# Kernel optimization log

Measured on AMD Instinct MI355X. Metric: run time of the kernel, lower is better.

Reference implementation:

```python
import jax, jax.numpy as jnp
import numpy as np

HIDDEN = 4096
HALF = HIDDEN // 2
THRESH = 0.85


def setup_inputs() -> dict:
    key = jax.random.key(0)
    ks = jax.random.split(key, 10)
    B, N, H = 8, 1024, HIDDEN
    s = lambda fan_in: 1.0 / np.sqrt(fan_in)
    return {
        "segment_embeddings": jax.random.normal(ks[0], (B, N, H), dtype=jnp.float32),
        "importance_scores": jax.random.uniform(ks[1], (B, N), dtype=jnp.float32),
        # similarity_proj: Linear(H, H/2) -> GELU -> LayerNorm(H/2)
        "W_sim": jax.random.uniform(ks[2], (H, HALF), jnp.float32, -s(H), s(H)),
        "b_sim": jnp.zeros((HALF,), jnp.float32),
        "ln_g": jnp.ones((HALF,), jnp.float32),
        "ln_b": jnp.zeros((HALF,), jnp.float32),
        # distill_head: Linear(H, H/2) -> GELU -> Linear(H/2, H)
        "W_d1": jax.random.uniform(ks[3], (H, HALF), jnp.float32, -s(H), s(H)),
        "b_d1": jnp.zeros((HALF,), jnp.float32),
        "W_d2": jax.random.uniform(ks[4], (HALF, H), jnp.float32, -s(HALF), s(HALF)),
        "b_d2": jnp.zeros((H,), jnp.float32),
    }


def _layer_norm(x, g, b, eps=1e-5):
    mu = jnp.mean(x, axis=-1, keepdims=True)
    var = jnp.var(x, axis=-1, keepdims=True)
    return (x - mu) * jax.lax.rsqrt(var + eps) * g + b


def _greedy_keep(sim, imp):
    """Sequential NMS-style suppression.
    kept[i]=0 iff exists j<i with kept[j]>0, sim[i,j]>thr, imp[j]>=imp[i]."""
    B, N, _ = sim.shape
    # cond[b,i,j]: pair (i,j) would suppress i if j still kept
    cond = (sim > THRESH) & (imp[:, None, :] >= imp[:, :, None])  # [B,N,N]
    idx = jnp.arange(N)

    def body(kept, i):
        valid = idx < i  # only j < i
        suppress = jnp.any(cond[:, i, :] & (kept > 0) & valid[None, :], axis=-1)
        kept = kept.at[:, i].set(jnp.where(suppress, 0.0, kept[:, i]))
        return kept, None

    kept, _ = jax.lax.scan(body, jnp.ones((B, N), sim.dtype), jnp.arange(1, N))
    return kept


def reference(segment_embeddings, importance_scores, W_sim, b_sim, ln_g, ln_b,
              W_d1, b_d1, W_d2, b_d2):
    # similarity projection
    p = jnp.einsum('bnh,hk->bnk', segment_embeddings, W_sim) + b_sim
    p = _layer_norm(jax.nn.gelu(p, approximate=False), ln_g, ln_b)
    norm = p / (jnp.linalg.norm(p, axis=-1, keepdims=True) + 1e-8)
    sim = jnp.einsum('bik,bjk->bij', norm, norm)  # [B,N,N]

    kept_mask = _greedy_keep(sim, importance_scores)

    weighted = segment_embeddings * importance_scores[..., None]
    h = jax.nn.gelu(jnp.einsum('bnh,hk->bnk', weighted, W_d1) + b_d1, approximate=False)
    compressed = jnp.einsum('bnk,kh->bnh', h, W_d2) + b_d2
    masked_compressed = compressed * kept_mask[..., None]
    return masked_compressed, kept_mask
```

## Files before the change

### kernel.cpp

```cpp
#include <hip/hip_runtime.h>

typedef __bf16 bf16_t;
typedef __attribute__((ext_vector_type(8))) __bf16 bf16x8;
typedef __attribute__((ext_vector_type(4))) float f32x4;

#define GLD16(gptr, lptr)                                                              \
  __builtin_amdgcn_global_load_lds((const __attribute__((address_space(1))) void*)(gptr), \
                                   (__attribute__((address_space(3))) void*)(lptr), 16, 0, 0)

#define BAR() __builtin_amdgcn_s_barrier()
#define WAIT_LGKM0()                                      \
  do {                                                    \
    asm volatile("s_waitcnt lgkmcnt(0)" ::: "memory");    \
    __builtin_amdgcn_sched_barrier(0);                    \
  } while (0)
#define WAIT_VM4() asm volatile("s_waitcnt vmcnt(4)" ::: "memory")
#define WAIT_VM0() asm volatile("s_waitcnt vmcnt(0)" ::: "memory")
#define PRIO1() __builtin_amdgcn_s_setprio(1)
#define PRIO0() __builtin_amdgcn_s_setprio(0)

__device__ __forceinline__ float gelu_f(float x) {
  return 0.5f * x * (1.0f + erff(x * 0.7071067811865476f));
}

__device__ __forceinline__ void ld_a4(bf16x8 (&a)[4][2], const char* b0, const char* b1) {
#pragma unroll
  for (int f = 0; f < 4; f++) {
    a[f][0] = *reinterpret_cast<const bf16x8*>(b0 + f * 2048);
    a[f][1] = *reinterpret_cast<const bf16x8*>(b1 + f * 2048);
  }
}

__device__ __forceinline__ void ld_b2(bf16x8 (&b)[2][2], const char* b0, const char* b1) {
#pragma unroll
  for (int f = 0; f < 2; f++) {
    b[f][0] = *reinterpret_cast<const bf16x8*>(b0 + f * 2048);
    b[f][1] = *reinterpret_cast<const bf16x8*>(b1 + f * 2048);
  }
}

template <int MH, int NH>
__device__ __forceinline__ void mm16(f32x4 (&acc)[8][4], const bf16x8 (&a)[4][2],
                                     const bf16x8 (&b)[2][2]) {
#pragma unroll
  for (int i = 0; i < 4; i++)
#pragma unroll
    for (int j = 0; j < 2; j++)
#pragma unroll
      for (int s = 0; s < 2; s++)
        acc[MH * 4 + i][NH * 2 + j] = __builtin_amdgcn_mfma_f32_16x16x32_bf16(
            a[i][s], b[j][s], acc[MH * 4 + i][NH * 2 + j], 0, 0, 0);
}

__device__ __forceinline__ void stage2(const bf16_t* src, char* ldst, size_t rowskip) {
  GLD16(src, ldst);
  GLD16(src + rowskip, ldst + 8192);
}

template <int EPI>
__global__ __launch_bounds__(512, 2) void gemm256(const bf16_t* __restrict__ A,
                                                  const bf16_t* __restrict__ BT,
                                                  float* __restrict__ C,
                                                  const float* __restrict__ bias,
                                                  const float* __restrict__ rowscale,
                                                  int M, int N, int K) {
  __shared__ char smem[131072];
  const int NKT = K >> 6;
  const int niter = NKT >> 1;

  const int nbn = N >> 8;
  int bid = blockIdx.x;
  const int cpx = gridDim.x >> 3;
  bid = (bid & 7) * cpx + (bid >> 3);
  const int m0 = (bid / nbn) << 8, n0 = (bid % nbn) << 8;

  const int t = threadIdx.x;
  const int lane = t & 63, wid = t >> 6;
  const int wr = wid >> 2, wc = wid & 3;
  const int fr = lane & 15, kq = lane >> 4;
  const int c0 = (kq ^ (fr & 7)) << 4;
  const int c1 = c0 ^ 64;

  const char* aB0 = smem + wr * 16384 + fr * 128 + c0;
  const char* aB1 = smem + wr * 16384 + fr * 128 + c1;
  const char* bB0 = smem + 65536 + (wc >> 1) * 16384 + ((wc & 1) * 64 + fr) * 128 + c0;
  const char* bB1 = smem + 65536 + (wc >> 1) * 16384 + ((wc & 1) * 64 + fr) * 128 + c1;

  const int sr0 = t >> 3;
  const int scol = ((t & 7) ^ (sr0 & 7)) * 8;
  const bf16_t* gA = A + (size_t)(m0 + sr0) * K + scol;
  const bf16_t* gB = BT + (size_t)(n0 + sr0) * K + scol;
  const size_t rskip = (size_t)64 * K;
  char* ldA = smem + t * 16;
  char* ldB = smem + 65536 + t * 16;

#define STG_A(kc, bb, h) stage2(gA + (size_t)(h)*128 * K + (size_t)(kc)*64, ldA + ((bb)*2 + (h)) * 16384, rskip)
#define STG_B(kc, bb, h) stage2(gB + (size_t)(h)*128 * K + (size_t)(kc)*64, ldB + ((bb)*2 + (h)) * 16384, rskip)

  f32x4 acc[8][4] = {};
  bf16x8 a[4][2], b0[2][2], b1[2][2];

  STG_B(0, 0, 0); STG_B(0, 0, 1); STG_A(0, 0, 0); STG_A(0, 0, 1);
  STG_B(1, 1, 0); STG_B(1, 1, 1);

  for (int it = 0; it < niter; ++it) {
    const int c1k = 2 * it + 1;
    const int c2k = (2 * it + 2 < NKT) ? 2 * it + 2 : NKT - 1;
    const int c3k = (2 * it + 3 < NKT) ? 2 * it + 3 : NKT - 1;

    WAIT_VM4();
    BAR();
    ld_a4(a, aB0, aB1);
    ld_b2(b0, bB0, bB1);
    STG_A(c1k, 1, 0);
    BAR(); WAIT_LGKM0();
    PRIO1(); mm16<0, 0>(acc, a, b0); PRIO0();
    BAR();
    ld_b2(b1, bB0 + 4096, bB1 + 4096);
    STG_A(c1k, 1, 1);
    BAR(); WAIT_LGKM0();
    PRIO1(); mm16<0, 1>(acc, a, b1); PRIO0();
    BAR();
    ld_a4(a, aB0 + 8192, aB1 + 8192);
    STG_B(c2k, 0, 0);
    BAR(); WAIT_LGKM0();
    PRIO1(); mm16<1, 0>(acc, a, b0); PRIO0();
    BAR();
    STG_B(c2k, 0, 1);
    BAR(); WAIT_LGKM0();
    PRIO1(); mm16<1, 1>(acc, a, b1); PRIO0();
    WAIT_VM4();
    BAR();
    ld_a4(a, aB0 + 32768, aB1 + 32768);
    ld_b2(b0, bB0 + 32768, bB1 + 32768);
    STG_A(c2k, 0, 0);
    BAR(); WAIT_LGKM0();
    PRIO1(); mm16<0, 0>(acc, a, b0); PRIO0();
    BAR();
    ld_b2(b1, bB0 + 36864, bB1 + 36864);
    STG_A(c2k, 0, 1);
    BAR(); WAIT_LGKM0();
    PRIO1(); mm16<0, 1>(acc, a, b1); PRIO0();
    BAR();
    ld_a4(a, aB0 + 40960, aB1 + 40960);
    STG_B(c3k, 1, 0);
    BAR(); WAIT_LGKM0();
    PRIO1(); mm16<1, 0>(acc, a, b0); PRIO0();
    BAR();
    STG_B(c3k, 1, 1);
    BAR(); WAIT_LGKM0();
    PRIO1(); mm16<1, 1>(acc, a, b1); PRIO0();
  }
  WAIT_VM0();

#undef STG_A
#undef STG_B

  const int r0 = kq * 4;
#pragma unroll
  for (int i = 0; i < 8; i++) {
    const int row = m0 + wr * 128 + i * 16 + r0;
#pragma unroll
    for (int j = 0; j < 4; j++) {
      const int col = n0 + wc * 64 + j * 16 + fr;
#pragma unroll
      for (int r = 0; r < 4; r++) {
        float v = acc[i][j][r];
        if (EPI == 1) v = (v + bias[col]) * rowscale[row + r];
        C[(size_t)(row + r) * N + col] = v;
      }
    }
  }
}

__global__ __launch_bounds__(256) void conv_bf16(const float* __restrict__ in,
                                                 bf16_t* __restrict__ out, int n8) {
  for (int idx = blockIdx.x * 256 + threadIdx.x; idx < n8; idx += gridDim.x * 256) {
    const float4* p = reinterpret_cast<const float4*>(in + (size_t)idx * 8);
    float4 a = p[0], b = p[1];
    bf16x8 v;
    v[0] = (bf16_t)a.x; v[1] = (bf16_t)a.y; v[2] = (bf16_t)a.z; v[3] = (bf16_t)a.w;
    v[4] = (bf16_t)b.x; v[5] = (bf16_t)b.y; v[6] = (bf16_t)b.z; v[7] = (bf16_t)b.w;
    *reinterpret_cast<bf16x8*>(out + (size_t)idx * 8) = v;
  }
}

__global__ __launch_bounds__(256) void transpose_conv(const float* __restrict__ src,
                                                      bf16_t* __restrict__ dst, int K,
                                                      int N, int dstStride) {
  __shared__ float lds[64][65];
  const int ntn = N >> 6;
  const int tile = blockIdx.x;
  const int tk = tile / ntn, tn = tile % ntn;
  const int k0 = tk << 6, n0 = tn << 6;
  const int t = threadIdx.x;
#pragma unroll
  for (int q = 0; q < 16; q++) {
    int idx = q * 256 + t;
    int kk = idx >> 6, nn = idx & 63;
    lds[kk][nn] = src[(size_t)(k0 + kk) * N + n0 + nn];
  }
  __syncthreads();
#pragma unroll
  for (int q = 0; q < 16; q++) {
    int idx = q * 256 + t;
    int nn = idx >> 6, kk = idx & 63;
    dst[(size_t)(n0 + nn) * dstStride + k0 + kk] = (bf16_t)lds[kk][nn];
  }
}

__global__ __launch_bounds__(256) void epilogue1(const float* __restrict__ X,
                                                 const float* __restrict__ imp,
                                                 const float* __restrict__ b_sim,
                                                 const float* __restrict__ ln_g,
                                                 const float* __restrict__ ln_b,
                                                 const float* __restrict__ b_d1,
                                                 bf16_t* __restrict__ Nrm,
                                                 bf16_t* __restrict__ Hbuf) {
  __shared__ float red[8];
  const int row = blockIdx.x;
  const int t = threadIdx.x;
  const int lane = t & 63, wid = t >> 6;
  const float* xr = X + (size_t)row * 4096;
  const int c0 = t * 8;

  float g[8];
  float s1 = 0.f, s2 = 0.f;
  {
    const float4* p = reinterpret_cast<const float4*>(xr + c0);
    float4 a = p[0], b = p[1];
    float xv[8] = {a.x, a.y, a.z, a.w, b.x, b.y, b.z, b.w};
#pragma unroll
    for (int q = 0; q < 8; q++) {
      float v = xv[q] + b_sim[c0 + q];
      float gv = gelu_f(v);
      g[q] = gv;
      s1 += gv;
      s2 += gv * gv;
    }
  }
#pragma unroll
  for (int o = 32; o > 0; o >>= 1) {
    s1 += __shfl_down(s1, o);
    s2 += __shfl_down(s2, o);
  }
  if (lane == 0) { red[wid] = s1; red[4 + wid] = s2; }
  __syncthreads();
  s1 = red[0] + red[1] + red[2] + red[3];
  s2 = red[4] + red[5] + red[6] + red[7];
  __syncthreads();

  const float mu = s1 * (1.0f / 2048.0f);
  const float var = s2 * (1.0f / 2048.0f) - mu * mu;
  const float rstd = rsqrtf(var + 1e-5f);

  float y[8];
  float s3 = 0.f;
#pragma unroll
  for (int q = 0; q < 8; q++) {
    float yv = (g[q] - mu) * rstd * ln_g[c0 + q] + ln_b[c0 + q];
    y[q] = yv;
    s3 += yv * yv;
  }
#pragma unroll
  for (int o = 32; o > 0; o >>= 1) s3 += __shfl_down(s3, o);
  if (lane == 0) red[wid] = s3;
  __syncthreads();
  s3 = red[0] + red[1] + red[2] + red[3];

  const float scale = 1.0f / (sqrtf(s3) + 1e-8f);
  bf16x8 nv;
#pragma unroll
  for (int q = 0; q < 8; q++) nv[q] = (bf16_t)(y[q] * scale);
  *reinterpret_cast<bf16x8*>(Nrm + (size_t)row * 2048 + c0) = nv;

  const float ir = imp[row];
  const float4* p2 = reinterpret_cast<const float4*>(xr + 2048 + c0);
  float4 a2 = p2[0], b2 = p2[1];
  float xv2[8] = {a2.x, a2.y, a2.z, a2.w, b2.x, b2.y, b2.z, b2.w};
  bf16x8 hv;
#pragma unroll
  for (int q = 0; q < 8; q++) {
    float v = xv2[q] * ir + b_d1[c0 + q];
    hv[q] = (bf16_t)gelu_f(v);
  }
  *reinterpret_cast<bf16x8*>(Hbuf + (size_t)row * 2048 + c0) = hv;
}

__global__ __launch_bounds__(256) void sim_gemm(const bf16_t* __restrict__ Nrm,
                                                const float* __restrict__ imp,
                                                unsigned long long* __restrict__ cond) {
  __shared__ bf16_t As[128 * 32];
  __shared__ bf16_t Bs[128 * 32];

  const int b = blockIdx.x / 36;
  const int tt = blockIdx.x % 36;
  int ti = 0;
  while ((ti + 1) * (ti + 2) / 2 <= tt) ti++;
  const int tj = tt - ti * (ti + 1) / 2;

  const bf16_t* Ab = Nrm + (size_t)b * 1024 * 2048;
  const int K = 2048;
  const int m0 = ti << 7, n0 = tj << 7;

  const int t = threadIdx.x;
  const int lane = t & 63, wid = t >> 6;
  const int wm = (wid >> 1) << 6, wn = (wid & 1) << 6;
  const int fr = lane & 15;
  const int krow = (lane >> 4) << 3;

  f32x4 acc[4][4] = {};

  const int sr = t >> 2;
  const int sc = (t & 3) << 3;
  const bf16_t* ga = Ab + (size_t)(m0 + sr) * K + sc;
  const bf16_t* gb = Ab + (size_t)(n0 + sr) * K + sc;
  bf16_t* lA0 = &As[wid * 512];
  bf16_t* lA1 = &As[2048 + wid * 512];
  bf16_t* lB0 = &Bs[wid * 512];
  bf16_t* lB1 = &Bs[2048 + wid * 512];
  const size_t rowskip = (size_t)64 * K;

  for (int k0 = 0; k0 < K; k0 += 32) {
    GLD16(ga + k0, lA0);
    GLD16(ga + rowskip + k0, lA1);
    GLD16(gb + k0, lB0);
    GLD16(gb + rowskip + k0, lB1);
    __syncthreads();
    bf16x8 af[4], bfr[4];
#pragma unroll
    for (int f = 0; f < 4; f++) {
      af[f] = *reinterpret_cast<const bf16x8*>(&As[(wm + f * 16 + fr) * 32 + krow]);
      bfr[f] = *reinterpret_cast<const bf16x8*>(&Bs[(wn + f * 16 + fr) * 32 + krow]);
    }
#pragma unroll
    for (int i = 0; i < 4; i++)
#pragma unroll
      for (int j = 0; j < 4; j++)
        acc[i][j] = __builtin_amdgcn_mfma_f32_16x16x32_bf16(af[i], bfr[j], acc[i][j], 0, 0, 0);
    __syncthreads();
  }

  const float* impb = imp + b * 1024;
  const int jw = (n0 + wn) >> 6;
  unsigned long long* crow = cond + (size_t)b * 1024 * 16;
  const int g = lane >> 4;
#pragma unroll
  for (int fm = 0; fm < 4; fm++) {
#pragma unroll
    for (int r = 0; r < 4; r++) {
      const int i = m0 + wm + fm * 16 + g * 4 + r;
      const float impi = impb[i];
      unsigned long long w0 = 0;
#pragma unroll
      for (int fn = 0; fn < 4; fn++) {
        const int j = n0 + wn + fn * 16 + fr;
        const float s = acc[fm][fn][r];
        const bool pred = (s > 0.85f) && (impb[j] >= impi) && (j < i);
        unsigned long long bal = __ballot(pred);
        w0 |= ((bal >> (g * 16)) & 0xFFFFull) << (fn * 16);
      }
      if (fr == 0) crow[(size_t)i * 16 + jw] = w0;
    }
  }
}

__global__ __launch_bounds__(256) void scan_keep(const unsigned long long* __restrict__ cond,
                                                 float* __restrict__ keptF,
                                                 float* __restrict__ outMask) {
  __shared__ unsigned long long kept[16];
  __shared__ unsigned char cand[1024];
  const int b = blockIdx.x;
  const int t = threadIdx.x;
  if (t < 16) kept[t] = ~0ull;
  const unsigned long long* cb = cond + (size_t)b * 1024 * 16;

  for (int i = t; i < 1024; i += 256) {
    const int wmax = i >> 6;
    unsigned long long any = 0;
    for (int w = 0; w < wmax; w++) any |= cb[i * 16 + w];
    const unsigned long long m = (i & 63) ? ((1ull << (i & 63)) - 1ull) : 0ull;
    any |= cb[i * 16 + wmax] & m;
    cand[i] = (any != 0);
  }
  __syncthreads();

  if (t < 64) {
    for (int i = 1; i < 1024; i++) {
      if (!cand[i]) continue;
      const int wmax = i >> 6;
      unsigned long long v = 0;
      if (t <= wmax) {
        const unsigned long long m =
            (t < wmax) ? ~0ull : ((i & 63) ? ((1ull << (i & 63)) - 1ull) : 0ull);
        v = cb[i * 16 + t] & kept[t] & m;
      }
      const bool sup = __any(v != 0);
      if (sup && t == 0) kept[i >> 6] &= ~(1ull << (i & 63));
    }
  }
  __syncthreads();

  for (int i = t; i < 1024; i += 256) {
    const float kv = ((kept[i >> 6] >> (i & 63)) & 1ull) ? 1.0f : 0.0f;
    keptF[b * 1024 + i] = kv;
    outMask[b * 1024 + i] = kv;
  }
}

extern "C" void kernel_launch(void* const* d_in, const int* in_sizes, int n_in,
                              void* d_out, int out_size, void* d_ws, size_t ws_size,
                              hipStream_t stream) {
  const float* seg = (const float*)d_in[0];
  const float* imp = (const float*)d_in[1];
  const float* Wsim = (const float*)d_in[2];
  const float* bsim = (const float*)d_in[3];
  const float* lng = (const float*)d_in[4];
  const float* lnb = (const float*)d_in[5];
  const float* Wd1 = (const float*)d_in[6];
  const float* bd1 = (const float*)d_in[7];
  const float* Wd2 = (const float*)d_in[8];
  const float* bd2 = (const float*)d_in[9];

  char* w = (char*)d_ws;
  bf16_t* A1 = (bf16_t*)w;  w += (size_t)8192 * 4096 * 2;
  bf16_t* W1T = (bf16_t*)w; w += (size_t)4096 * 4096 * 2;
  bf16_t* W2T = (bf16_t*)w; w += (size_t)4096 * 2048 * 2;
  bf16_t* Nrm = (bf16_t*)w; w += (size_t)8192 * 2048 * 2;
  bf16_t* Hb = (bf16_t*)w;  w += (size_t)8192 * 2048 * 2;
  unsigned long long* cond = (unsigned long long*)w; w += (size_t)8 * 1024 * 16 * 8;
  float* keptF = (float*)w; w += (size_t)8192 * 4;

  float* X = (float*)d_out;
  float* outMask = (float*)d_out + (size_t)8192 * 4096;

  conv_bf16<<<4096, 256, 0, stream>>>(seg, A1, 8192 * 512);
  transpose_conv<<<2048, 256, 0, stream>>>(Wsim, W1T, 4096, 2048, 4096);
  transpose_conv<<<2048, 256, 0, stream>>>(Wd1, W1T + (size_t)2048 * 4096, 4096, 2048, 4096);
  transpose_conv<<<2048, 256, 0, stream>>>(Wd2, W2T, 2048, 4096, 2048);

  gemm256<0><<<512, 512, 0, stream>>>(A1, W1T, X, nullptr, nullptr, 8192, 4096, 4096);
  epilogue1<<<8192, 256, 0, stream>>>(X, imp, bsim, lng, lnb, bd1, Nrm, Hb);
  sim_gemm<<<288, 256, 0, stream>>>(Nrm, imp, cond);
  scan_keep<<<8, 256, 0, stream>>>(cond, keptF, outMask);
  gemm256<1><<<512, 512, 0, stream>>>(Hb, W2T, (float*)d_out, bd2, keptF, 8192, 4096, 2048);
}
```

Before: 838.1 us.

## Software-pipeline LDS fragment loads in GEMM and store intermediate projection as bf16

The GEMM main loop is reordered so each MFMA block runs before the next global-to-LDS stage and LDS fragment loads are issued. The first fragments are preloaded before the loop, which drops about half the barriers and uses a vmcnt(2) wait instead of vmcnt(4). The first GEMM now writes its output as bf16 instead of fp32, halving the intermediate write and the epilogue read traffic. The cost is extra rounding before GELU, LayerNorm and the similarity threshold, which could flip borderline keep decisions. The reordered wait counts also carry a risk of LDS hazards.

```diff
diff --git a/kernel.cpp b/kernel.cpp
--- a/kernel.cpp
+++ b/kernel.cpp
@@ -14,6 +14,7 @@
     asm volatile("s_waitcnt lgkmcnt(0)" ::: "memory");    \
     __builtin_amdgcn_sched_barrier(0);                    \
   } while (0)
+#define WAIT_VM2() asm volatile("s_waitcnt vmcnt(2)" ::: "memory")
 #define WAIT_VM4() asm volatile("s_waitcnt vmcnt(4)" ::: "memory")
 #define WAIT_VM0() asm volatile("s_waitcnt vmcnt(0)" ::: "memory")
 #define PRIO1() __builtin_amdgcn_s_setprio(1)
@@ -102,54 +103,58 @@
 
   STG_B(0, 0, 0); STG_B(0, 0, 1); STG_A(0, 0, 0); STG_A(0, 0, 1);
   STG_B(1, 1, 0); STG_B(1, 1, 1);
+  WAIT_VM4();
+  BAR();
+  ld_a4(a, aB0, aB1);
+  ld_b2(b0, bB0, bB1);
 
   for (int it = 0; it < niter; ++it) {
     const int c1k = 2 * it + 1;
     const int c2k = (2 * it + 2 < NKT) ? 2 * it + 2 : NKT - 1;
     const int c3k = (2 * it + 3 < NKT) ? 2 * it + 3 : NKT - 1;
 
-    WAIT_VM4();
-    BAR();
+    WAIT_LGKM0();
+    PRIO1(); mm16<0, 0>(acc, a, b0); PRIO0();
+    STG_A(c1k, 1, 0);
+    ld_b2(b1, bB0 + 4096, bB1 + 4096);
+    BAR();
+    WAIT_LGKM0();
+    PRIO1(); mm16<0, 1>(acc, a, b1); PRIO0();
+    STG_A(c1k, 1, 1);
+    ld_a4(a, aB0 + 8192, aB1 + 8192);
+    BAR();
+    WAIT_LGKM0();
+    PRIO1(); mm16<1, 0>(acc, a, b0); PRIO0();
+    STG_B(c2k, 0, 0);
+    WAIT_VM2();
+    BAR();
+    WAIT_LGKM0();
+    PRIO1(); mm16<1, 1>(acc, a, b1); PRIO0();
+    STG_B(c2k, 0, 1);
+    ld_a4(a, aB0 + 32768, aB1 + 32768);
+    ld_b2(b0, bB0 + 32768, bB1 + 32768);
+    BAR();
+    WAIT_LGKM0();
+    PRIO1(); mm16<0, 0>(acc, a, b0); PRIO0();
+    STG_A(c2k, 0, 0);
+    ld_b2(b1, bB0 + 36864, bB1 + 36864);
+    BAR();
+    WAIT_LGKM0();
+    PRIO1(); mm16<0, 1>(acc, a, b1); PRIO0();
+    STG_A(c2k, 0, 1);
+    ld_a4(a, aB0 + 40960, aB1 + 40960);
+    BAR();
+    WAIT_LGKM0();
+    PRIO1(); mm16<1, 0>(acc, a, b0); PRIO0();
+    STG_B(c3k, 1, 0);
+    WAIT_VM2();
+    BAR();
+    WAIT_LGKM0();
+    PRIO1(); mm16<1, 1>(acc, a, b1); PRIO0();
+    STG_B(c3k, 1, 1);
     ld_a4(a, aB0, aB1);
     ld_b2(b0, bB0, bB1);
-    STG_A(c1k, 1, 0);
-    BAR(); WAIT_LGKM0();
-    PRIO1(); mm16<0, 0>(acc, a, b0); PRIO0();
-    BAR();
-    ld_b2(b1, bB0 + 4096, bB1 + 4096);
-    STG_A(c1k, 1, 1);
-    BAR(); WAIT_LGKM0();
-    PRIO1(); mm16<0, 1>(acc, a, b1); PRIO0();
-    BAR();
-    ld_a4(a, aB0 + 8192, aB1 + 8192);
-    STG_B(c2k, 0, 0);
-    BAR(); WAIT_LGKM0();
-    PRIO1(); mm16<1, 0>(acc, a, b0); PRIO0();
-    BAR();
-    STG_B(c2k, 0, 1);
-    BAR(); WAIT_LGKM0();
-    PRIO1(); mm16<1, 1>(acc, a, b1); PRIO0();
-    WAIT_VM4();
-    BAR();
-    ld_a4(a, aB0 + 32768, aB1 + 32768);
-    ld_b2(b0, bB0 + 32768, bB1 + 32768);
-    STG_A(c2k, 0, 0);
-    BAR(); WAIT_LGKM0();
-    PRIO1(); mm16<0, 0>(acc, a, b0); PRIO0();
-    BAR();
-    ld_b2(b1, bB0 + 36864, bB1 + 36864);
-    STG_A(c2k, 0, 1);
-    BAR(); WAIT_LGKM0();
-    PRIO1(); mm16<0, 1>(acc, a, b1); PRIO0();
-    BAR();
-    ld_a4(a, aB0 + 40960, aB1 + 40960);
-    STG_B(c3k, 1, 0);
-    BAR(); WAIT_LGKM0();
-    PRIO1(); mm16<1, 0>(acc, a, b0); PRIO0();
-    BAR();
-    STG_B(c3k, 1, 1);
-    BAR(); WAIT_LGKM0();
-    PRIO1(); mm16<1, 1>(acc, a, b1); PRIO0();
+    BAR();
   }
   WAIT_VM0();
 
@@ -166,8 +171,12 @@
 #pragma unroll
       for (int r = 0; r < 4; r++) {
         float v = acc[i][j][r];
-        if (EPI == 1) v = (v + bias[col]) * rowscale[row + r];
-        C[(size_t)(row + r) * N + col] = v;
+        if (EPI == 1) {
+          v = (v + bias[col]) * rowscale[row + r];
+          C[(size_t)(row + r) * N + col] = v;
+        } else {
+          reinterpret_cast<bf16_t*>(C)[(size_t)(row + r) * N + col] = (bf16_t)v;
+        }
       }
     }
   }
@@ -209,7 +218,7 @@
   }
 }
 
-__global__ __launch_bounds__(256) void epilogue1(const float* __restrict__ X,
+__global__ __launch_bounds__(256) void epilogue1(const bf16_t* __restrict__ X,
                                                  const float* __restrict__ imp,
                                                  const float* __restrict__ b_sim,
                                                  const float* __restrict__ ln_g,
@@ -221,18 +230,16 @@
   const int row = blockIdx.x;
   const int t = threadIdx.x;
   const int lane = t & 63, wid = t >> 6;
-  const float* xr = X + (size_t)row * 4096;
+  const bf16_t* xr = X + (size_t)row * 4096;
   const int c0 = t * 8;
 
   float g[8];
   float s1 = 0.f, s2 = 0.f;
   {
-    const float4* p = reinterpret_cast<const float4*>(xr + c0);
-    float4 a = p[0], b = p[1];
-    float xv[8] = {a.x, a.y, a.z, a.w, b.x, b.y, b.z, b.w};
+    bf16x8 xv = *reinterpret_cast<const bf16x8*>(xr + c0);
 #pragma unroll
     for (int q = 0; q < 8; q++) {
-      float v = xv[q] + b_sim[c0 + q];
+      float v = (float)xv[q] + b_sim[c0 + q];
       float gv = gelu_f(v);
       g[q] = gv;
       s1 += gv;
@@ -275,13 +282,11 @@
   *reinterpret_cast<bf16x8*>(Nrm + (size_t)row * 2048 + c0) = nv;
 
   const float ir = imp[row];
-  const float4* p2 = reinterpret_cast<const float4*>(xr + 2048 + c0);
-  float4 a2 = p2[0], b2 = p2[1];
-  float xv2[8] = {a2.x, a2.y, a2.z, a2.w, b2.x, b2.y, b2.z, b2.w};
+  bf16x8 xv2 = *reinterpret_cast<const bf16x8*>(xr + 2048 + c0);
   bf16x8 hv;
 #pragma unroll
   for (int q = 0; q < 8; q++) {
-    float v = xv2[q] * ir + b_d1[c0 + q];
+    float v = (float)xv2[q] * ir + b_d1[c0 + q];
     hv[q] = (bf16_t)gelu_f(v);
   }
   *reinterpret_cast<bf16x8*>(Hbuf + (size_t)row * 2048 + c0) = hv;
@@ -431,7 +436,7 @@
   unsigned long long* cond = (unsigned long long*)w; w += (size_t)8 * 1024 * 16 * 8;
   float* keptF = (float*)w; w += (size_t)8192 * 4;
 
-  float* X = (float*)d_out;
+  bf16_t* Xb = (bf16_t*)d_out;
   float* outMask = (float*)d_out + (size_t)8192 * 4096;
 
   conv_bf16<<<4096, 256, 0, stream>>>(seg, A1, 8192 * 512);
@@ -439,8 +444,8 @@
   transpose_conv<<<2048, 256, 0, stream>>>(Wd1, W1T + (size_t)2048 * 4096, 4096, 2048, 4096);
   transpose_conv<<<2048, 256, 0, stream>>>(Wd2, W2T, 2048, 4096, 2048);
 
-  gemm256<0><<<512, 512, 0, stream>>>(A1, W1T, X, nullptr, nullptr, 8192, 4096, 4096);
-  epilogue1<<<8192, 256, 0, stream>>>(X, imp, bsim, lng, lnb, bd1, Nrm, Hb);
+  gemm256<2><<<512, 512, 0, stream>>>(A1, W1T, (float*)Xb, nullptr, nullptr, 8192, 4096, 4096);
+  epilogue1<<<8192, 256, 0, stream>>>(Xb, imp, bsim, lng, lnb, bd1, Nrm, Hb);
   sim_gemm<<<288, 256, 0, stream>>>(Nrm, imp, cond);
   scan_keep<<<8, 256, 0, stream>>>(cond, keptF, outMask);
   gemm256<1><<<512, 512, 0, stream>>>(Hb, W2T, (float*)d_out, bd2, keptF, 8192, 4096, 2048);
```

New measurement: 828.7 us. Within noise of the previous version (-1.1%).
